# Optimization experiments

Measured on AMD Instinct MI355X. Metric: run time of the kernel, lower is better.

## Reference

```python
import jax, jax.numpy as jnp
import numpy as np

SIGMA = 25.0
N, E, F, D = 10000, 160000, 256, 3


def setup_inputs() -> dict:
    key = jax.random.key(0)
    ks = jax.random.split(key, 24)
    s = 0.02
    inp = {
        "x": jax.random.normal(ks[0], (N, D), jnp.float32),
        "edge_index": jax.random.randint(ks[1], (2, E), 0, N, jnp.int64),
        "t": jax.random.uniform(ks[2], (N, 1), jnp.float32, 1e-3, 1.0),
        "emb_pcs": jax.random.normal(ks[3], (N, F), jnp.float32),
        # x_encoder
        "enc_W": jax.random.normal(ks[4], (D, F), jnp.float32) * s,
        "enc_b": jnp.zeros((F,), jnp.float32),
        # GaussianFourierProjection (scale=30, fixed) + Linear
        "fourier_W": jax.random.normal(ks[5], (F // 2,), jnp.float32) * 30.0,
        "te_W": jax.random.normal(ks[6], (F, F), jnp.float32) * s,
        "te_b": jnp.zeros((F,), jnp.float32),
        # mlp1 / mlp2: Linear(6F,F) -> ReLU -> Linear(F,F)
        "m1_W1": jax.random.normal(ks[7], (6 * F, F), jnp.float32) * s,
        "m1_b1": jnp.zeros((F,), jnp.float32),
        "m1_W2": jax.random.normal(ks[8], (F, F), jnp.float32) * s,
        "m1_b2": jnp.zeros((F,), jnp.float32),
        "m2_W1": jax.random.normal(ks[9], (6 * F, F), jnp.float32) * s,
        "m2_b1": jnp.zeros((F,), jnp.float32),
        "m2_W2": jax.random.normal(ks[10], (F, F), jnp.float32) * s,
        "m2_b2": jnp.zeros((F,), jnp.float32),
        # mlp3: Linear(6F,F) -> ReLU -> Linear(F,D)
        "m3_W1": jax.random.normal(ks[11], (6 * F, F), jnp.float32) * s,
        "m3_b1": jnp.zeros((F,), jnp.float32),
        "m3_W2": jax.random.normal(ks[12], (F, D), jnp.float32) * s,
        "m3_b2": jnp.zeros((D,), jnp.float32),
    }
    return inp


def _edge_conv(h, src, dst, W1, b1, W2, b2, n):
    # PyG EdgeConv: out_i = max_{j->i} MLP([x_i, x_j - x_i])
    hi = h[dst]                                             # [E, 3F]
    e = jnp.concatenate([hi, h[src] - hi], axis=-1)         # [E, 6F]
    e = jax.nn.relu(e @ W1 + b1) @ W2 + b2                  # [E, out]
    out = jax.ops.segment_max(e, dst, num_segments=n)
    return jnp.where(jnp.isfinite(out), out, 0.0)           # empty segments -> 0


def reference(x, edge_index, t, emb_pcs,
              enc_W, enc_b, fourier_W, te_W, te_b,
              m1_W1, m1_b1, m1_W2, m1_b2,
              m2_W1, m2_b1, m2_W2, m2_b2,
              m3_W1, m3_b1, m3_W2, m3_b2):
    src, dst = edge_index[0], edge_index[1]
    n = x.shape[0]
    # time embedding: Fourier projection -> Linear -> swish
    tv = t[:, 0]
    proj = tv[:, None] * fourier_W[None, :] * (2.0 * np.pi)  # [N, F/2]
    temb = jnp.concatenate([jnp.sin(proj), jnp.cos(proj)], axis=-1) @ te_W + te_b
    temb = temb * jax.nn.sigmoid(temb)                       # [N, F]
    h = x @ enc_W + enc_b                                    # [N, F]
    h = jnp.concatenate([h, temb, emb_pcs], axis=-1)         # [N, 3F]
    h = jax.nn.relu(_edge_conv(h, src, dst, m1_W1, m1_b1, m1_W2, m1_b2, n))
    h = jnp.concatenate([h, temb, emb_pcs], axis=-1)
    h = jax.nn.relu(_edge_conv(h, src, dst, m2_W1, m2_b1, m2_W2, m2_b2, n))
    h = jnp.concatenate([h, temb, emb_pcs], axis=-1)
    h = _edge_conv(h, src, dst, m3_W1, m3_b1, m3_W2, m3_b2, n)  # [N, D]
    # marginal_prob_std(t) = sqrt((sigma^(2t) - 1) / (2 ln sigma))
    std = jnp.sqrt((jnp.power(SIGMA, 2.0 * t) - 1.0) / (2.0 * jnp.log(SIGMA)))
    return h / (std + 1e-7)
```

## Files before the change

### kernel.cpp

```cpp
#include <hip/hip_runtime.h>
#include <hip/hip_bf16.h>
#include <math.h>

#define HC 768
#define DPB 8

typedef __attribute__((ext_vector_type(8))) short bf16x8;
typedef __attribute__((ext_vector_type(4))) float f32x4;

__device__ __forceinline__ float bf2f(unsigned short h) {
    return __uint_as_float(((unsigned)h) << 16);
}
__device__ __forceinline__ unsigned short f2bf(float f) {
    unsigned u = __float_as_uint(f);
    return (unsigned short)((u + 0x7fffu + ((u >> 16) & 1u)) >> 16);
}
__device__ __forceinline__ unsigned pack_bf2(float a, float b) {
    __hip_bfloat162 h = __float22bfloat162_rn(make_float2(a, b));
    return *reinterpret_cast<unsigned*>(&h);
}

__device__ __forceinline__ unsigned enc_f(float f) {
    unsigned u = __float_as_uint(f);
    return (u & 0x80000000u) ? ~u : (u | 0x80000000u);
}
__device__ __forceinline__ float dec_f(unsigned e) {
    unsigned u = (e & 0x80000000u) ? (e & 0x7FFFFFFFu) : ~e;
    return __uint_as_float(u);
}
#define ENC_NEG_INF 0x007FFFFFu

__global__ void precompute_kernel(const float* __restrict__ x,
                                  const float* __restrict__ t,
                                  const float* __restrict__ emb,
                                  const float* __restrict__ enc_W,
                                  const float* __restrict__ enc_b,
                                  const float* __restrict__ fw,
                                  const float* __restrict__ te_W,
                                  const float* __restrict__ te_b,
                                  unsigned short* __restrict__ hcat,
                                  float* __restrict__ invstd,
                                  int N) {
    __shared__ float ti[8][256];
    __shared__ float tv[8];
    const int n0 = blockIdx.x * 8;
    const int tid = threadIdx.x;

    if (tid < 8) {
        int n = n0 + tid;
        float tt = (n < N) ? t[n] : 1.0f;
        tv[tid] = tt;
        const float ln_s = 3.2188758248682006f;
        float p = expf(2.0f * tt * ln_s);
        float sd = sqrtf((p - 1.0f) / (2.0f * ln_s));
        if (n < N) invstd[n] = 1.0f / (sd + 1e-7f);
    }
    __syncthreads();

    const float TWO_PI = 6.283185307179586f;
    for (int p = tid; p < 8 * 128; p += 256) {
        int n = p >> 7, j = p & 127;
        float pr = tv[n] * fw[j] * TWO_PI;
        ti[n][j]       = sinf(pr);
        ti[n][j + 128] = cosf(pr);
    }
    __syncthreads();

    const int j = tid;
    float acc[8];
#pragma unroll
    for (int n = 0; n < 8; ++n) acc[n] = 0.f;
    for (int k = 0; k < 256; ++k) {
        float w = te_W[k * 256 + j];
#pragma unroll
        for (int n = 0; n < 8; ++n) acc[n] += ti[n][k] * w;
    }
    float bj  = te_b[j];
    float ew0 = enc_W[0 * 256 + j], ew1 = enc_W[1 * 256 + j], ew2 = enc_W[2 * 256 + j];
    float ebj = enc_b[j];
    for (int n = 0; n < 8; ++n) {
        int node = n0 + n;
        if (node >= N) break;
        float v = acc[n] + bj;
        float temb = v / (1.0f + expf(-v));
        float h0 = x[node * 3 + 0] * ew0 + x[node * 3 + 1] * ew1 +
                   x[node * 3 + 2] * ew2 + ebj;
        hcat[(size_t)node * HC + j]       = f2bf(h0);
        hcat[(size_t)node * HC + 256 + j] = f2bf(temb);
        hcat[(size_t)node * HC + 512 + j] = f2bf(emb[node * 256 + j]);
    }
}

__global__ void prep_all_kernel(const float* __restrict__ W1a,
                                const float* __restrict__ W1b,
                                const float* __restrict__ W1c,
                                const float* __restrict__ W2a,
                                const float* __restrict__ W2b,
                                const float* __restrict__ W2c,
                                unsigned short* __restrict__ WcatT,
                                unsigned short* __restrict__ W2T,
                                unsigned short* __restrict__ W2T3) {
    __shared__ float buf[64][65];
    const int bid = blockIdx.x;
    const int tid = threadIdx.x;
    const int tx = tid & 63, ty = tid >> 6;

    if (bid < 288) {
        const int l = bid / 96, r = bid - l * 96;
        const float* W1 = (l == 0) ? W1a : (l == 1) ? W1b : W1c;
        unsigned short* WT = WcatT + (size_t)l * 512 * 768;
        const int k0 = (r % 12) * 64, n0 = (r / 12) * 64;
#pragma unroll
        for (int i = 0; i < 16; ++i) {
            int kl = ty + i * 4;
            int k = k0 + kl, n = n0 + tx;
            float v = (n < 256) ? (W1[(size_t)k * 256 + n] - W1[(size_t)(k + 768) * 256 + n])
                                : W1[(size_t)(k + 768) * 256 + (n - 256)];
            buf[kl][tx] = v;
        }
        __syncthreads();
#pragma unroll
        for (int i = 0; i < 16; ++i) {
            int nl = ty + i * 4;
            WT[(size_t)(n0 + nl) * 768 + k0 + tx] = f2bf(buf[tx][nl]);
        }
    } else if (bid < 320) {
        const int m = bid - 288, l = m >> 4, r = m & 15;
        const float* W2 = (l == 0) ? W2a : W2b;
        unsigned short* WT = W2T + (size_t)l * 256 * 256;
        const int k0 = (r & 3) * 64, n0 = (r >> 2) * 64;
#pragma unroll
        for (int i = 0; i < 16; ++i) {
            int kl = ty + i * 4;
            buf[kl][tx] = W2[(size_t)(k0 + kl) * 256 + n0 + tx];
        }
        __syncthreads();
#pragma unroll
        for (int i = 0; i < 16; ++i) {
            int nl = ty + i * 4;
            WT[(size_t)(n0 + nl) * 256 + k0 + tx] = f2bf(buf[tx][nl]);
        }
    } else {
        int idx = (bid - 320) * 256 + tid;
        int n = idx >> 8, k = idx & 255;
        W2T3[idx] = (n < 3) ? f2bf(W2c[(size_t)k * 3 + n]) : (unsigned short)0;
    }
}

__global__ __launch_bounds__(256)
void node_gemm_mfma_kernel(const unsigned short* __restrict__ A,
                           const unsigned short* __restrict__ BT,
                           const float* __restrict__ b1,
                           unsigned short* __restrict__ C,
                           int M) {
    const int row0 = blockIdx.x * 64, col0 = blockIdx.y * 64;
    const int tid = threadIdx.x;
    const int wv = tid >> 6, lane = tid & 63;
    const int q = lane >> 4, nl = lane & 15;

    int row = row0 + wv * 16 + nl;
    int rowc = (row < M) ? row : (M - 1);
    const unsigned short* pa = A + (size_t)rowc * HC + q * 8;

    f32x4 acc[4];
#pragma unroll
    for (int t = 0; t < 4; ++t) acc[t] = (f32x4){0.f, 0.f, 0.f, 0.f};

    for (int ks = 0; ks < 24; ++ks) {
        const int k0 = ks * 32;
        const bf16x8 av = *(const bf16x8*)(pa + k0);
#pragma unroll
        for (int t = 0; t < 4; ++t) {
            const bf16x8 bv = *(const bf16x8*)(BT + (size_t)(col0 + t * 16 + nl) * 768 + k0 + q * 8);
            acc[t] = __builtin_amdgcn_mfma_f32_16x16x32_bf16(av, bv, acc[t], 0, 0, 0);
        }
    }

    const int r0 = row0 + wv * 16 + q * 4;
#pragma unroll
    for (int t = 0; t < 4; ++t) {
        int col = col0 + t * 16 + nl;
        float bb = (col < 256) ? b1[col] : 0.f;
#pragma unroll
        for (int i = 0; i < 4; ++i) {
            int r = r0 + i;
            if (r < M) C[(size_t)r * 512 + col] = f2bf(acc[t][i] + bb);
        }
    }
}

__global__ void zero_u32_kernel(unsigned* __restrict__ p, int count) {
    int idx = blockIdx.x * 256 + threadIdx.x;
    if (idx < count) p[idx] = 0u;
}
__global__ void hist_kernel(const int* __restrict__ dst, unsigned* __restrict__ cnt, int E) {
    int e = blockIdx.x * 256 + threadIdx.x;
    if (e < E) atomicAdd(&cnt[dst[e]], 1u);
}
__global__ void scan_kernel(const unsigned* __restrict__ cnt,
                            int* __restrict__ row_start, int N) {
    __shared__ unsigned buf[1024];
    __shared__ unsigned carry;
    const int tid = threadIdx.x;
    if (tid == 0) carry = 0u;
    __syncthreads();
    for (int base = 0; base < N; base += 1024) {
        int i = base + tid;
        unsigned v = (i < N) ? cnt[i] : 0u;
        buf[tid] = v;
        __syncthreads();
#pragma unroll
        for (int off = 1; off < 1024; off <<= 1) {
            unsigned add = (tid >= off) ? buf[tid - off] : 0u;
            __syncthreads();
            buf[tid] += add;
            __syncthreads();
        }
        if (i < N) row_start[i] = (int)(carry + buf[tid] - v);
        __syncthreads();
        if (tid == 0) carry += buf[1023];
        __syncthreads();
    }
    if (tid == 0) row_start[N] = (int)carry;
}
__global__ void scatter_kernel(const int* __restrict__ src, const int* __restrict__ dst,
                               const int* __restrict__ row_start,
                               unsigned* __restrict__ wcnt,
                               int* __restrict__ es, int* __restrict__ ed, int E) {
    int e = blockIdx.x * 256 + threadIdx.x;
    if (e >= E) return;
    int d = dst[e];
    int pos = row_start[d] + (int)atomicAdd(&wcnt[d], 1u);
    es[pos] = src[e];
    ed[pos] = d;
}

__global__ __launch_bounds__(256, 3)
void edge_seg_gemm_kernel(const unsigned short* __restrict__ RQb,
                          const int* __restrict__ es,
                          const int* __restrict__ ed,
                          const int* __restrict__ row_start,
                          const unsigned short* __restrict__ W2T,
                          const float* __restrict__ b2,
                          unsigned short* __restrict__ hcat,
                          int N, int E) {
    __shared__ unsigned short af[64][264];
    __shared__ unsigned short rdst[DPB][256];
    __shared__ unsigned lseg[DPB * 256];
    __shared__ int ss[64], sdl[64];
    const int d0 = blockIdx.x * DPB;
    const int tid = threadIdx.x;
    const int wv = tid >> 6, lane = tid & 63;
    const int q = lane >> 4, nl = lane & 15;

    for (int i = tid; i < DPB * 256; i += 256) lseg[i] = ENC_NEG_INF;

    {
        int rrow = tid >> 5;
        int kc = (tid & 31) * 8;
        int d = d0 + rrow;
        int dc = (d < N) ? d : (N - 1);
        *(bf16x8*)&rdst[rrow][kc] = *(const bf16x8*)(RQb + (size_t)dc * 512 + kc);
    }

    const int eBeg = row_start[d0];
    const int eEnd = row_start[min(d0 + DPB, N)];

    for (int c0 = eBeg; c0 < eEnd; c0 += 64) {
        __syncthreads();
        if (tid < 64) {
            int e = c0 + tid;
            ss[tid]  = (e < eEnd) ? es[e] : 0;
            sdl[tid] = (e < eEnd) ? (ed[e] - d0) : -1;
        }
        __syncthreads();

        {
            const int el = tid >> 2;
            const int kc = (tid & 3) * 64;
            int dl = sdl[el];
            int dla = (dl >= 0) ? dl : 0;
            int srow = ss[el];
            const unsigned short* ps = RQb + (size_t)srow * 512 + 256 + kc;
#pragma unroll
            for (int j = 0; j < 8; ++j) {
                bf16x8 dv = *(const bf16x8*)&rdst[dla][kc + j * 8];
                bf16x8 sv = *(const bf16x8*)(ps + j * 8);
                float f[8];
#pragma unroll
                for (int u = 0; u < 8; ++u)
                    f[u] = fmaxf(bf2f((unsigned short)dv[u]) + bf2f((unsigned short)sv[u]), 0.f);
                uint4 o;
                o.x = pack_bf2(f[0], f[1]);
                o.y = pack_bf2(f[2], f[3]);
                o.z = pack_bf2(f[4], f[5]);
                o.w = pack_bf2(f[6], f[7]);
                *(uint4*)&af[el][kc + j * 8] = o;
            }
        }
        __syncthreads();

#pragma unroll
        for (int sub = 0; sub < 4; ++sub) {
            f32x4 acc[4];
#pragma unroll
            for (int t = 0; t < 4; ++t) acc[t] = (f32x4){0.f, 0.f, 0.f, 0.f};
#pragma unroll
            for (int ks = 0; ks < 8; ++ks) {
                const bf16x8 av = *(const bf16x8*)&af[sub * 16 + nl][ks * 32 + q * 8];
#pragma unroll
                for (int t = 0; t < 4; ++t) {
                    const bf16x8 bv = *(const bf16x8*)(W2T +
                        (size_t)(wv * 64 + t * 16 + nl) * 256 + ks * 32 + q * 8);
                    acc[t] = __builtin_amdgcn_mfma_f32_16x16x32_bf16(av, bv, acc[t], 0, 0, 0);
                }
            }
            const int m0 = sub * 16 + q * 4;
            int dls[4];
#pragma unroll
            for (int i = 0; i < 4; ++i) dls[i] = sdl[m0 + i];
#pragma unroll
            for (int t = 0; t < 4; ++t) {
                const int col = wv * 64 + t * 16 + nl;
                float cur = -INFINITY;
                int cd = dls[0];
#pragma unroll
                for (int i = 0; i < 4; ++i) {
                    int dl = dls[i];
                    if (dl != cd) {
                        if (cd >= 0) atomicMax(&lseg[cd * 256 + col], enc_f(cur));
                        cur = -INFINITY; cd = dl;
                    }
                    cur = fmaxf(cur, acc[t][i]);
                }
                if (cd >= 0) atomicMax(&lseg[cd * 256 + col], enc_f(cur));
            }
        }
    }
    __syncthreads();

    for (int i = tid; i < DPB * 256; i += 256) {
        int dl = i >> 8, col = i & 255;
        int d = d0 + dl;
        if (d >= N) continue;
        float f = dec_f(lseg[i]);
        float v = isfinite(f) ? fmaxf(f + b2[col], 0.f) : 0.f;
        hcat[(size_t)d * HC + col] = f2bf(v);
    }
}

__global__ __launch_bounds__(256)
void edge3_mfma_kernel(const unsigned short* __restrict__ RQb,
                       const int* __restrict__ es,
                       const int* __restrict__ ed,
                       const unsigned short* __restrict__ W2T3,
                       const float* __restrict__ b2,
                       unsigned* __restrict__ seg3,
                       int E) {
    const int wave = blockIdx.x * 4 + (threadIdx.x >> 6);
    const int lane = threadIdx.x & 63;
    const int q = lane >> 4, nl = lane & 15;
    const int e0 = wave * 16;
    if (e0 >= E) return;

    bf16x8 bv[8];
#pragma unroll
    for (int ks = 0; ks < 8; ++ks)
        bv[ks] = *(const bf16x8*)(W2T3 + (size_t)nl * 256 + ks * 32 + q * 8);

    int eA = e0 + nl;
    int eAc = (eA < E) ? eA : (E - 1);
    const int dA = ed[eAc], sA = es[eAc];
    const unsigned short* pd = RQb + (size_t)dA * 512 + q * 8;
    const unsigned short* ps = RQb + (size_t)sA * 512 + 256 + q * 8;

    f32x4 acc = (f32x4){0.f, 0.f, 0.f, 0.f};
#pragma unroll
    for (int ks = 0; ks < 8; ++ks) {
        bf16x8 dv = *(const bf16x8*)(pd + ks * 32);
        bf16x8 sv = *(const bf16x8*)(ps + ks * 32);
        float f[8];
#pragma unroll
        for (int u = 0; u < 8; ++u)
            f[u] = fmaxf(bf2f((unsigned short)dv[u]) + bf2f((unsigned short)sv[u]), 0.f);
        uint4 o;
        o.x = pack_bf2(f[0], f[1]);
        o.y = pack_bf2(f[2], f[3]);
        o.z = pack_bf2(f[4], f[5]);
        o.w = pack_bf2(f[6], f[7]);
        bf16x8 av = *(bf16x8*)&o;
        acc = __builtin_amdgcn_mfma_f32_16x16x32_bf16(av, bv[ks], acc, 0, 0, 0);
    }

    if (nl < 3) {
        float bb = b2[nl];
        float cur = -INFINITY;
        int cd = -2;
#pragma unroll
        for (int i = 0; i < 4; ++i) {
            int e = e0 + q * 4 + i;
            int d = (e < E) ? ed[e] : -1;
            if (d != cd) {
                if (cd >= 0) atomicMax(&seg3[(size_t)cd * 3 + nl], enc_f(cur + bb));
                cur = -INFINITY; cd = d;
            }
            if (d >= 0) cur = fmaxf(cur, acc[i]);
        }
        if (cd >= 0) atomicMax(&seg3[(size_t)cd * 3 + nl], enc_f(cur + bb));
    }
}

__global__ void seg_init_kernel(unsigned* __restrict__ seg, int count) {
    int idx = blockIdx.x * 256 + threadIdx.x;
    if (idx < count) seg[idx] = ENC_NEG_INF;
}
__global__ void finalize3_kernel(const unsigned* __restrict__ seg3,
                                 const float* __restrict__ invstd,
                                 float* __restrict__ out, int N) {
    int idx = blockIdx.x * 256 + threadIdx.x;
    if (idx >= N * 3) return;
    int n = idx / 3;
    float f = dec_f(seg3[idx]);
    if (!isfinite(f)) f = 0.f;
    out[idx] = f * invstd[n];
}

extern "C" void kernel_launch(void* const* d_in, const int* in_sizes, int n_in,
                              void* d_out, int out_size, void* d_ws, size_t ws_size,
                              hipStream_t stream) {
    const float* x     = (const float*)d_in[0];
    const int*   ei    = (const int*)d_in[1];
    const float* t     = (const float*)d_in[2];
    const float* emb   = (const float*)d_in[3];
    const float* enc_W = (const float*)d_in[4];
    const float* enc_b = (const float*)d_in[5];
    const float* fw    = (const float*)d_in[6];
    const float* te_W  = (const float*)d_in[7];
    const float* te_b  = (const float*)d_in[8];
    const float* W1[3] = {(const float*)d_in[9],  (const float*)d_in[13], (const float*)d_in[17]};
    const float* b1[3] = {(const float*)d_in[10], (const float*)d_in[14], (const float*)d_in[18]};
    const float* W2[3] = {(const float*)d_in[11], (const float*)d_in[15], (const float*)d_in[19]};
    const float* b2[3] = {(const float*)d_in[12], (const float*)d_in[16], (const float*)d_in[20]};

    const int N = in_sizes[2];
    const int E = in_sizes[1] / 2;
    const int* src = ei;
    const int* dst = ei + E;

    char* ws = (char*)d_ws;
    unsigned short* hcat  = (unsigned short*)ws; ws += (size_t)N * HC * 2;
    unsigned short* RQb   = (unsigned short*)ws; ws += (size_t)N * 512 * 2;
    unsigned short* WcatT = (unsigned short*)ws; ws += (size_t)3 * 512 * 768 * 2;
    unsigned short* W2T   = (unsigned short*)ws; ws += (size_t)2 * 256 * 256 * 2;
    unsigned short* W2T3  = (unsigned short*)ws; ws += (size_t)16 * 256 * 2;
    unsigned* seg3        = (unsigned*)ws;       ws += (size_t)N * 3 * 4;
    float*    invstd      = (float*)ws;          ws += (size_t)N * 4;
    int*      es          = (int*)ws;            ws += (size_t)E * 4;
    int*      ed          = (int*)ws;            ws += (size_t)E * 4;
    unsigned* cnt         = (unsigned*)ws;       ws += (size_t)N * 4;
    unsigned* wcnt        = (unsigned*)ws;       ws += (size_t)N * 4;
    int*      row_start   = (int*)ws;            ws += (size_t)(N + 1) * 4;

    zero_u32_kernel<<<(2 * N + 255) / 256, 256, 0, stream>>>(cnt, 2 * N);
    hist_kernel<<<(E + 255) / 256, 256, 0, stream>>>(dst, cnt, E);
    scan_kernel<<<1, 1024, 0, stream>>>(cnt, row_start, N);
    scatter_kernel<<<(E + 255) / 256, 256, 0, stream>>>(src, dst, row_start, wcnt, es, ed, E);

    precompute_kernel<<<(N + 7) / 8, 256, 0, stream>>>(
        x, t, emb, enc_W, enc_b, fw, te_W, te_b, hcat, invstd, N);

    prep_all_kernel<<<336, 256, 0, stream>>>(W1[0], W1[1], W1[2], W2[0], W2[1], W2[2],
                                             WcatT, W2T, W2T3);
    seg_init_kernel<<<(N * 3 + 255) / 256, 256, 0, stream>>>(seg3, N * 3);

    for (int l = 0; l < 3; ++l) {
        dim3 gn((N + 63) / 64, 8);
        node_gemm_mfma_kernel<<<gn, 256, 0, stream>>>(
            hcat, WcatT + (size_t)l * 512 * 768, b1[l], RQb, N);
        if (l < 2) {
            edge_seg_gemm_kernel<<<(N + DPB - 1) / DPB, 256, 0, stream>>>(
                RQb, es, ed, row_start, W2T + (size_t)l * 256 * 256, b2[l], hcat, N, E);
        } else {
            int chunks = (E + 15) / 16;
            edge3_mfma_kernel<<<(chunks + 3) / 4, 256, 0, stream>>>(
                RQb, es, ed, W2T3, b2[l], seg3, E);
            finalize3_kernel<<<(N * 3 + 255) / 256, 256, 0, stream>>>(seg3, invstd, (float*)d_out, N);
        }
    }
}
```

Measured before the change: 559.7 us.

## Merge setup kernels and halve edge chunk to raise occupancy

Merges the node precompute and weight-prep kernels into one launch, and folds the count-zeroing and seg3 init into a single init kernel, cutting launch count. The edge segment GEMM now processes 32 edges per chunk instead of 64, which halves the A-tile shared memory so the launch bound can go from 3 to 4 blocks per SM. Each wave now issues two MFMA rows per B load to reuse B fragments. The trade-off is more chunk iterations and syncs per destination block, plus reduced register headroom under the tighter launch bound.

```diff
diff --git a/kernel.cpp b/kernel.cpp
--- a/kernel.cpp
+++ b/kernel.cpp
@@ -30,120 +30,122 @@
 }
 #define ENC_NEG_INF 0x007FFFFFu
 
-__global__ void precompute_kernel(const float* __restrict__ x,
-                                  const float* __restrict__ t,
-                                  const float* __restrict__ emb,
-                                  const float* __restrict__ enc_W,
-                                  const float* __restrict__ enc_b,
-                                  const float* __restrict__ fw,
-                                  const float* __restrict__ te_W,
-                                  const float* __restrict__ te_b,
-                                  unsigned short* __restrict__ hcat,
-                                  float* __restrict__ invstd,
-                                  int N) {
-    __shared__ float ti[8][256];
-    __shared__ float tv[8];
-    const int n0 = blockIdx.x * 8;
+__global__ void pre_and_prep_kernel(const float* __restrict__ x,
+                                    const float* __restrict__ t,
+                                    const float* __restrict__ emb,
+                                    const float* __restrict__ enc_W,
+                                    const float* __restrict__ enc_b,
+                                    const float* __restrict__ fw,
+                                    const float* __restrict__ te_W,
+                                    const float* __restrict__ te_b,
+                                    unsigned short* __restrict__ hcat,
+                                    float* __restrict__ invstd,
+                                    const float* __restrict__ W1a,
+                                    const float* __restrict__ W1b,
+                                    const float* __restrict__ W1c,
+                                    const float* __restrict__ W2a,
+                                    const float* __restrict__ W2b,
+                                    const float* __restrict__ W2c,
+                                    unsigned short* __restrict__ WcatT,
+                                    unsigned short* __restrict__ W2T,
+                                    unsigned short* __restrict__ W2T3,
+                                    int N, int nPre) {
+    __shared__ float smem[64 * 65];
     const int tid = threadIdx.x;
 
-    if (tid < 8) {
-        int n = n0 + tid;
-        float tt = (n < N) ? t[n] : 1.0f;
-        tv[tid] = tt;
-        const float ln_s = 3.2188758248682006f;
-        float p = expf(2.0f * tt * ln_s);
-        float sd = sqrtf((p - 1.0f) / (2.0f * ln_s));
-        if (n < N) invstd[n] = 1.0f / (sd + 1e-7f);
-    }
-    __syncthreads();
-
-    const float TWO_PI = 6.283185307179586f;
-    for (int p = tid; p < 8 * 128; p += 256) {
-        int n = p >> 7, j = p & 127;
-        float pr = tv[n] * fw[j] * TWO_PI;
-        ti[n][j]       = sinf(pr);
-        ti[n][j + 128] = cosf(pr);
-    }
-    __syncthreads();
-
-    const int j = tid;
-    float acc[8];
-#pragma unroll
-    for (int n = 0; n < 8; ++n) acc[n] = 0.f;
-    for (int k = 0; k < 256; ++k) {
-        float w = te_W[k * 256 + j];
-#pragma unroll
-        for (int n = 0; n < 8; ++n) acc[n] += ti[n][k] * w;
-    }
-    float bj  = te_b[j];
-    float ew0 = enc_W[0 * 256 + j], ew1 = enc_W[1 * 256 + j], ew2 = enc_W[2 * 256 + j];
-    float ebj = enc_b[j];
-    for (int n = 0; n < 8; ++n) {
-        int node = n0 + n;
-        if (node >= N) break;
-        float v = acc[n] + bj;
-        float temb = v / (1.0f + expf(-v));
-        float h0 = x[node * 3 + 0] * ew0 + x[node * 3 + 1] * ew1 +
-                   x[node * 3 + 2] * ew2 + ebj;
-        hcat[(size_t)node * HC + j]       = f2bf(h0);
-        hcat[(size_t)node * HC + 256 + j] = f2bf(temb);
-        hcat[(size_t)node * HC + 512 + j] = f2bf(emb[node * 256 + j]);
-    }
-}
-
-__global__ void prep_all_kernel(const float* __restrict__ W1a,
-                                const float* __restrict__ W1b,
-                                const float* __restrict__ W1c,
-                                const float* __restrict__ W2a,
-                                const float* __restrict__ W2b,
-                                const float* __restrict__ W2c,
-                                unsigned short* __restrict__ WcatT,
-                                unsigned short* __restrict__ W2T,
-                                unsigned short* __restrict__ W2T3) {
-    __shared__ float buf[64][65];
-    const int bid = blockIdx.x;
-    const int tid = threadIdx.x;
-    const int tx = tid & 63, ty = tid >> 6;
-
-    if (bid < 288) {
-        const int l = bid / 96, r = bid - l * 96;
-        const float* W1 = (l == 0) ? W1a : (l == 1) ? W1b : W1c;
-        unsigned short* WT = WcatT + (size_t)l * 512 * 768;
-        const int k0 = (r % 12) * 64, n0 = (r / 12) * 64;
-#pragma unroll
-        for (int i = 0; i < 16; ++i) {
-            int kl = ty + i * 4;
-            int k = k0 + kl, n = n0 + tx;
-            float v = (n < 256) ? (W1[(size_t)k * 256 + n] - W1[(size_t)(k + 768) * 256 + n])
-                                : W1[(size_t)(k + 768) * 256 + (n - 256)];
-            buf[kl][tx] = v;
-        }
-        __syncthreads();
-#pragma unroll
-        for (int i = 0; i < 16; ++i) {
-            int nl = ty + i * 4;
-            WT[(size_t)(n0 + nl) * 768 + k0 + tx] = f2bf(buf[tx][nl]);
-        }
-    } else if (bid < 320) {
-        const int m = bid - 288, l = m >> 4, r = m & 15;
-        const float* W2 = (l == 0) ? W2a : W2b;
-        unsigned short* WT = W2T + (size_t)l * 256 * 256;
-        const int k0 = (r & 3) * 64, n0 = (r >> 2) * 64;
-#pragma unroll
-        for (int i = 0; i < 16; ++i) {
-            int kl = ty + i * 4;
-            buf[kl][tx] = W2[(size_t)(k0 + kl) * 256 + n0 + tx];
-        }
-        __syncthreads();
-#pragma unroll
-        for (int i = 0; i < 16; ++i) {
-            int nl = ty + i * 4;
-            WT[(size_t)(n0 + nl) * 256 + k0 + tx] = f2bf(buf[tx][nl]);
+    if ((int)blockIdx.x < nPre) {
+        float (*ti)[256] = (float(*)[256])smem;
+        float* tv = smem + 8 * 256;
+        const int n0 = blockIdx.x * 8;
+
+        if (tid < 8) {
+            int n = n0 + tid;
+            float tt = (n < N) ? t[n] : 1.0f;
+            tv[tid] = tt;
+            const float ln_s = 3.2188758248682006f;
+            float p = expf(2.0f * tt * ln_s);
+            float sd = sqrtf((p - 1.0f) / (2.0f * ln_s));
+            if (n < N) invstd[n] = 1.0f / (sd + 1e-7f);
+        }
+        __syncthreads();
+
+        const float TWO_PI = 6.283185307179586f;
+        for (int p = tid; p < 8 * 128; p += 256) {
+            int n = p >> 7, j = p & 127;
+            float pr = tv[n] * fw[j] * TWO_PI;
+            ti[n][j]       = sinf(pr);
+            ti[n][j + 128] = cosf(pr);
+        }
+        __syncthreads();
+
+        const int j = tid;
+        float acc[8];
+#pragma unroll
+        for (int n = 0; n < 8; ++n) acc[n] = 0.f;
+        for (int k = 0; k < 256; ++k) {
+            float w = te_W[k * 256 + j];
+#pragma unroll
+            for (int n = 0; n < 8; ++n) acc[n] += ti[n][k] * w;
+        }
+        float bj  = te_b[j];
+        float ew0 = enc_W[0 * 256 + j], ew1 = enc_W[1 * 256 + j], ew2 = enc_W[2 * 256 + j];
+        float ebj = enc_b[j];
+        for (int n = 0; n < 8; ++n) {
+            int node = n0 + n;
+            if (node >= N) break;
+            float v = acc[n] + bj;
+            float temb = v / (1.0f + expf(-v));
+            float h0 = x[node * 3 + 0] * ew0 + x[node * 3 + 1] * ew1 +
+                       x[node * 3 + 2] * ew2 + ebj;
+            hcat[(size_t)node * HC + j]       = f2bf(h0);
+            hcat[(size_t)node * HC + 256 + j] = f2bf(temb);
+            hcat[(size_t)node * HC + 512 + j] = f2bf(emb[node * 256 + j]);
         }
     } else {
-        int idx = (bid - 320) * 256 + tid;
-        int n = idx >> 8, k = idx & 255;
-        W2T3[idx] = (n < 3) ? f2bf(W2c[(size_t)k * 3 + n]) : (unsigned short)0;
+        float (*buf)[65] = (float(*)[65])smem;
+        const int bid = blockIdx.x - nPre;
+        const int tx = tid & 63, ty = tid >> 6;
+
+        if (bid < 288) {
+            const int l = bid / 96, r = bid - l * 96;
+            const float* W1 = (l == 0) ? W1a : (l == 1) ? W1b : W1c;
+            unsigned short* WT = WcatT + (size_t)l * 512 * 768;
+            const int k0 = (r % 12) * 64, n0 = (r / 12) * 64;
+#pragma unroll
+            for (int i = 0; i < 16; ++i) {
+                int kl = ty + i * 4;
+                int k = k0 + kl, n = n0 + tx;
+                float v = (n < 256) ? (W1[(size_t)k * 256 + n] - W1[(size_t)(k + 768) * 256 + n])
+                                    : W1[(size_t)(k + 768) * 256 + (n - 256)];
+                buf[kl][tx] = v;
+            }
+            __syncthreads();
+#pragma unroll
+            for (int i = 0; i < 16; ++i) {
+                int nl = ty + i * 4;
+                WT[(size_t)(n0 + nl) * 768 + k0 + tx] = f2bf(buf[tx][nl]);
+            }
+        } else if (bid < 320) {
+            const int m = bid - 288, l = m >> 4, r = m & 15;
+            const float* W2 = (l == 0) ? W2a : W2b;
+            unsigned short* WT = W2T + (size_t)l * 256 * 256;
+            const int k0 = (r & 3) * 64, n0 = (r >> 2) * 64;
+#pragma unroll
+            for (int i = 0; i < 16; ++i) {
+                int kl = ty + i * 4;
+                buf[kl][tx] = W2[(size_t)(k0 + kl) * 256 + n0 + tx];
+            }
+            __syncthreads();
+#pragma unroll
+            for (int i = 0; i < 16; ++i) {
+                int nl = ty + i * 4;
+                WT[(size_t)(n0 + nl) * 256 + k0 + tx] = f2bf(buf[tx][nl]);
+            }
+        } else {
+            int idx = (bid - 320) * 256 + tid;
+            int n = idx >> 8, k = idx & 255;
+            W2T3[idx] = (n < 3) ? f2bf(W2c[(size_t)k * 3 + n]) : (unsigned short)0;
+        }
     }
 }
 
@@ -189,9 +191,10 @@
     }
 }
 
-__global__ void zero_u32_kernel(unsigned* __restrict__ p, int count) {
+__global__ void init_kernel(unsigned* __restrict__ cnt, unsigned* __restrict__ seg3, int N) {
     int idx = blockIdx.x * 256 + threadIdx.x;
-    if (idx < count) p[idx] = 0u;
+    if (idx < 2 * N) cnt[idx] = 0u;
+    else if (idx < 5 * N) seg3[idx - 2 * N] = ENC_NEG_INF;
 }
 __global__ void hist_kernel(const int* __restrict__ dst, unsigned* __restrict__ cnt, int E) {
     int e = blockIdx.x * 256 + threadIdx.x;
@@ -235,7 +238,7 @@
     ed[pos] = d;
 }
 
-__global__ __launch_bounds__(256, 3)
+__global__ __launch_bounds__(256, 4)
 void edge_seg_gemm_kernel(const unsigned short* __restrict__ RQb,
                           const int* __restrict__ es,
                           const int* __restrict__ ed,
@@ -244,10 +247,10 @@
                           const float* __restrict__ b2,
                           unsigned short* __restrict__ hcat,
                           int N, int E) {
-    __shared__ unsigned short af[64][264];
+    __shared__ unsigned short af[32][264];
     __shared__ unsigned short rdst[DPB][256];
     __shared__ unsigned lseg[DPB * 256];
-    __shared__ int ss[64], sdl[64];
+    __shared__ int ss[32], sdl[32];
     const int d0 = blockIdx.x * DPB;
     const int tid = threadIdx.x;
     const int wv = tid >> 6, lane = tid & 63;
@@ -266,9 +269,9 @@
     const int eBeg = row_start[d0];
     const int eEnd = row_start[min(d0 + DPB, N)];
 
-    for (int c0 = eBeg; c0 < eEnd; c0 += 64) {
-        __syncthreads();
-        if (tid < 64) {
+    for (int c0 = eBeg; c0 < eEnd; c0 += 32) {
+        __syncthreads();
+        if (tid < 32) {
             int e = c0 + tid;
             ss[tid]  = (e < eEnd) ? es[e] : 0;
             sdl[tid] = (e < eEnd) ? (ed[e] - d0) : -1;
@@ -276,16 +279,17 @@
         __syncthreads();
 
         {
-            const int el = tid >> 2;
-            const int kc = (tid & 3) * 64;
+            const int el = tid >> 3;
+            const int ksl = tid & 7;
             int dl = sdl[el];
             int dla = (dl >= 0) ? dl : 0;
             int srow = ss[el];
-            const unsigned short* ps = RQb + (size_t)srow * 512 + 256 + kc;
-#pragma unroll
-            for (int j = 0; j < 8; ++j) {
-                bf16x8 dv = *(const bf16x8*)&rdst[dla][kc + j * 8];
-                bf16x8 sv = *(const bf16x8*)(ps + j * 8);
+            const unsigned short* ps = RQb + (size_t)srow * 512 + 256;
+#pragma unroll
+            for (int j = 0; j < 4; ++j) {
+                const int k = ksl * 8 + j * 64;
+                bf16x8 dv = *(const bf16x8*)&rdst[dla][k];
+                bf16x8 sv = *(const bf16x8*)(ps + k);
                 float f[8];
 #pragma unroll
                 for (int u = 0; u < 8; ++u)
@@ -295,26 +299,32 @@
                 o.y = pack_bf2(f[2], f[3]);
                 o.z = pack_bf2(f[4], f[5]);
                 o.w = pack_bf2(f[6], f[7]);
-                *(uint4*)&af[el][kc + j * 8] = o;
-            }
-        }
-        __syncthreads();
-
-#pragma unroll
-        for (int sub = 0; sub < 4; ++sub) {
-            f32x4 acc[4];
-#pragma unroll
-            for (int t = 0; t < 4; ++t) acc[t] = (f32x4){0.f, 0.f, 0.f, 0.f};
-#pragma unroll
-            for (int ks = 0; ks < 8; ++ks) {
-                const bf16x8 av = *(const bf16x8*)&af[sub * 16 + nl][ks * 32 + q * 8];
-#pragma unroll
-                for (int t = 0; t < 4; ++t) {
-                    const bf16x8 bv = *(const bf16x8*)(W2T +
-                        (size_t)(wv * 64 + t * 16 + nl) * 256 + ks * 32 + q * 8);
-                    acc[t] = __builtin_amdgcn_mfma_f32_16x16x32_bf16(av, bv, acc[t], 0, 0, 0);
-                }
-            }
+                *(uint4*)&af[el][k] = o;
+            }
+        }
+        __syncthreads();
+
+        f32x4 acc[2][4];
+#pragma unroll
+        for (int s = 0; s < 2; ++s)
+#pragma unroll
+            for (int t = 0; t < 4; ++t) acc[s][t] = (f32x4){0.f, 0.f, 0.f, 0.f};
+
+#pragma unroll
+        for (int ks = 0; ks < 8; ++ks) {
+            const bf16x8 av0 = *(const bf16x8*)&af[nl][ks * 32 + q * 8];
+            const bf16x8 av1 = *(const bf16x8*)&af[16 + nl][ks * 32 + q * 8];
+#pragma unroll
+            for (int t = 0; t < 4; ++t) {
+                const bf16x8 bv = *(const bf16x8*)(W2T +
+                    (size_t)(wv * 64 + t * 16 + nl) * 256 + ks * 32 + q * 8);
+                acc[0][t] = __builtin_amdgcn_mfma_f32_16x16x32_bf16(av0, bv, acc[0][t], 0, 0, 0);
+                acc[1][t] = __builtin_amdgcn_mfma_f32_16x16x32_bf16(av1, bv, acc[1][t], 0, 0, 0);
+            }
+        }
+
+#pragma unroll
+        for (int sub = 0; sub < 2; ++sub) {
             const int m0 = sub * 16 + q * 4;
             int dls[4];
 #pragma unroll
@@ -331,7 +341,7 @@
                         if (cd >= 0) atomicMax(&lseg[cd * 256 + col], enc_f(cur));
                         cur = -INFINITY; cd = dl;
                     }
-                    cur = fmaxf(cur, acc[t][i]);
+                    cur = fmaxf(cur, acc[sub][t][i]);
                 }
                 if (cd >= 0) atomicMax(&lseg[cd * 256 + col], enc_f(cur));
             }
@@ -410,10 +420,6 @@
     }
 }
 
-__global__ void seg_init_kernel(unsigned* __restrict__ seg, int count) {
-    int idx = blockIdx.x * 256 + threadIdx.x;
-    if (idx < count) seg[idx] = ENC_NEG_INF;
-}
 __global__ void finalize3_kernel(const unsigned* __restrict__ seg3,
                                  const float* __restrict__ invstd,
                                  float* __restrict__ out, int N) {
@@ -461,17 +467,15 @@
     unsigned* wcnt        = (unsigned*)ws;       ws += (size_t)N * 4;
     int*      row_start   = (int*)ws;            ws += (size_t)(N + 1) * 4;
 
-    zero_u32_kernel<<<(2 * N + 255) / 256, 256, 0, stream>>>(cnt, 2 * N);
+    init_kernel<<<(5 * N + 255) / 256, 256, 0, stream>>>(cnt, seg3, N);
     hist_kernel<<<(E + 255) / 256, 256, 0, stream>>>(dst, cnt, E);
     scan_kernel<<<1, 1024, 0, stream>>>(cnt, row_start, N);
     scatter_kernel<<<(E + 255) / 256, 256, 0, stream>>>(src, dst, row_start, wcnt, es, ed, E);
 
-    precompute_kernel<<<(N + 7) / 8, 256, 0, stream>>>(
-        x, t, emb, enc_W, enc_b, fw, te_W, te_b, hcat, invstd, N);
-
-    prep_all_kernel<<<336, 256, 0, stream>>>(W1[0], W1[1], W1[2], W2[0], W2[1], W2[2],
-                                             WcatT, W2T, W2T3);
-    seg_init_kernel<<<(N * 3 + 255) / 256, 256, 0, stream>>>(seg3, N * 3);
+    const int nPre = (N + 7) / 8;
+    pre_and_prep_kernel<<<nPre + 336, 256, 0, stream>>>(
+        x, t, emb, enc_W, enc_b, fw, te_W, te_b, hcat, invstd,
+        W1[0], W1[1], W1[2], W2[0], W2[1], W2[2], WcatT, W2T, W2T3, N, nPre);
 
     for (int l = 0; l < 3; ++l) {
         dim3 gn((N + 63) / 64, 8);
```

Result: slower. 645.5 us (+15.3%).
